# Kernel optimization log

Hardware: AMD Instinct MI355X
Metric: run time of the kernel (lower is better)

The kernel has to match this reference:

```python
import jax, jax.numpy as jnp
import numpy as np

B, T, L = 256, 1024, 64
INIT = 0.1


def setup_inputs() -> dict:
    key = jax.random.key(0)
    k1, k2, k3, k4, k5 = jax.random.split(key, 5)
    scores = jax.random.normal(k1, (B, T, L), dtype=jnp.float32)
    targets = jax.random.randint(k2, (B, T), 0, L)
    start = jax.random.uniform(k3, (L,), dtype=jnp.float32, minval=-INIT, maxval=INIT)
    T_mat = jax.random.uniform(k4, (L, L), dtype=jnp.float32, minval=-INIT, maxval=INIT)
    end = jax.random.uniform(k5, (L,), dtype=jnp.float32, minval=-INIT, maxval=INIT)
    return {"scores": scores, "targets": targets, "start": start, "T_mat": T_mat, "end": end}


def reference(scores, targets, start, T_mat, end):
    # scores: [B,T,L], targets: [B,T] int, start/end: [L], T_mat: [L,L] with T_mat[cur, prev]
    Ttr = T_mat.T  # [prev, cur]

    # --- normalizers via forward algorithm (scan over time) ---
    prev0 = start[None, :] + scores[:, 0]  # [B,L]

    def step(prev, emit):  # prev [B,L], emit [B,L]
        cur = prev[:, :, None] + emit[:, None, :] + Ttr[None, :, :]  # [B,prev,cur]
        return jax.scipy.special.logsumexp(cur, axis=1), None

    emits_t = jnp.swapaxes(scores, 0, 1)[1:]  # [T-1,B,L]
    prev, _ = jax.lax.scan(step, prev0, emits_t)
    normalizers = jax.scipy.special.logsumexp(prev + end[None, :], axis=1)  # [B]

    # --- gold path score ---
    emits = jnp.take_along_axis(scores, targets[:, :, None], axis=2).squeeze(2).sum(axis=1)  # [B]
    trans = (start[targets[:, 0]]
             + T_mat[targets[:, 1:], targets[:, :-1]].sum(axis=1)
             + end[targets[:, -1]])  # [B]
    target_scores = emits + trans

    return (normalizers - target_scores).mean()
```

## Files before the change

### kernel.cpp

```cpp
#include <hip/hip_runtime.h>

#define NB 256
#define NT 1024
#define NL 64

typedef __fp16 h2v __attribute__((ext_vector_type(2)));

__device__ __forceinline__ float rfl_f(float v) {
  return __builtin_bit_cast(float, __builtin_amdgcn_readfirstlane(__builtin_bit_cast(int, v)));
}

__device__ __forceinline__ float dpp_xor1(float v) {
  int i = __builtin_bit_cast(int, v);
  int r = __builtin_amdgcn_update_dpp(i, i, 0xB1, 0xF, 0xF, false);
  return __builtin_bit_cast(float, r);
}

#define DOT4(P, B)                                                            \
  s0 = __builtin_amdgcn_fdot2(__builtin_bit_cast(h2v, (P).x), Rh[(B) + 0], s0, false); \
  s1 = __builtin_amdgcn_fdot2(__builtin_bit_cast(h2v, (P).y), Rh[(B) + 1], s1, false); \
  s2 = __builtin_amdgcn_fdot2(__builtin_bit_cast(h2v, (P).z), Rh[(B) + 2], s2, false); \
  s3 = __builtin_amdgcn_fdot2(__builtin_bit_cast(h2v, (P).w), Rh[(B) + 3], s3, false);

#define CRF_STEP(EF)                                                          \
  do {                                                                        \
    float wn = dpp_xor1(w);                                                   \
    h2v pk = __builtin_amdgcn_cvt_pkrtz(w, wn);                               \
    lb[wslot] = __builtin_bit_cast(int, pk);                                  \
    int4 P0 = lbv[0], P1 = lbv[1], P2 = lbv[2], P3 = lbv[3];                  \
    int4 P4 = lbv[4], P5 = lbv[5], P6 = lbv[6], P7 = lbv[7];                  \
    int e5 = (P0.x >> 10) & 0x1f;                                             \
    float K = __builtin_bit_cast(float, (130 - e5) << 23);                    \
    float KE = K * (EF);                                                      \
    e2 += e5 - 3;                                                             \
    float s0 = 0.f, s1 = 0.f, s2 = 0.f, s3 = 0.f;                             \
    DOT4(P0, 0); DOT4(P1, 4); DOT4(P2, 8); DOT4(P3, 12);                      \
    DOT4(P4, 16); DOT4(P5, 20); DOT4(P6, 24); DOT4(P7, 28);                   \
    w = ((s0 + s1) + (s2 + s3)) * KE;                                         \
  } while (0)

#define AQ __ATOMIC_ACQUIRE
#define RL __ATOMIC_RELEASE
#define SCOPE __HIP_MEMORY_SCOPE_AGENT

__global__ __launch_bounds__(64) void fb_kernel(const float* __restrict__ scores,
                                                const int* __restrict__ targets,
                                                const float* __restrict__ start,
                                                const float* __restrict__ Tm,
                                                const float* __restrict__ endv,
                                                float* __restrict__ wsA,
                                                float* __restrict__ wsG,
                                                float* __restrict__ wsL,
                                                int* __restrict__ flagF,
                                                int* __restrict__ flagG,
                                                int* __restrict__ flagL,
                                                float* __restrict__ out) {
  const int lane = threadIdx.x;
  const int bb = blockIdx.x;

  if (bb >= 2 * NB) {
    const int b = bb - 2 * NB;
    const int* tg = targets + b * NT;
    const float* sc = scores + (size_t)b * NT * NL;
    float acc = 0.f;
    for (int t = lane; t < NT; t += 64) {
      int c = tg[t];
      acc += sc[t * NL + c];
      if (t > 0) acc += Tm[c * NL + tg[t - 1]];
    }
#pragma unroll
    for (int off = 32; off > 0; off >>= 1) acc += __shfl_xor(acc, off, 64);
    if (lane == 0) wsG[b] = acc + start[tg[0]] + endv[tg[NT - 1]];
    __threadfence();
    if (lane == 0) __hip_atomic_store(&flagG[b], 1, RL, SCOPE);
    return;
  }

  __shared__ int4 lbv_s[16];
  int* lb = (int*)lbv_s;
  const int4* lbv = lbv_s;
  const int wslot = (lane & 1) * 32 + (lane >> 1);

  const bool bwd = bb >= NB;
  const int b = bwd ? bb - NB : bb;
  const float* sc = scores + (size_t)b * NT * NL;
  const float LN2 = 0.69314718055994530942f;

  const float* Tb = bwd ? (Tm + lane) : (Tm + lane * NL);
  const int str = bwd ? NL : 1;
  h2v Rh[32];
#pragma unroll
  for (int k = 0; k < 32; k++)
    Rh[k] = __builtin_amdgcn_cvt_pkrtz(__expf(Tb[(2 * k) * str]),
                                       __expf(Tb[(2 * k + 1) * str]));

  if (!bwd) {
    float a0 = start[lane] + sc[lane];
    float m0 = rfl_f(a0);
    float w = __expf(a0 - m0) * 16.f;
    int e2 = -4;

    float buf[4];
#pragma unroll
    for (int k = 0; k < 4; k++) buf[k] = sc[(1 + k) * NL + lane];

    for (int i = 0; i < 128; i++) {
      float nb4[4];
      int tb = 5 + 4 * i;
#pragma unroll
      for (int k = 0; k < 4; k++) nb4[k] = sc[(tb + k) * NL + lane];
      float Ev[4];
#pragma unroll
      for (int k = 0; k < 4; k++) Ev[k] = __expf(buf[k]);
      CRF_STEP(Ev[0]);
      CRF_STEP(Ev[1]);
      CRF_STEP(Ev[2]);
      CRF_STEP(Ev[3]);
#pragma unroll
      for (int k = 0; k < 4; k++) buf[k] = nb4[k];
    }
    wsA[b * NL + lane] = m0 + (float)e2 * LN2 + __logf(w);
    __threadfence();
    if (lane == 0) __hip_atomic_store(&flagF[b], 1, RL, SCOPE);
  } else {
    float a0 = endv[lane] + sc[(NT - 1) * NL + lane];
    float m0 = rfl_f(a0);
    float w = __expf(a0 - m0) * 16.f;
    int e2 = -4;

    float buf[4];
#pragma unroll
    for (int k = 0; k < 4; k++) buf[k] = sc[(1022 - k) * NL + lane];

    for (int i = 0; i < 127; i++) {
      float nb4[4];
      int tb = 1018 - 4 * i;
#pragma unroll
      for (int k = 0; k < 4; k++) nb4[k] = sc[(tb - k) * NL + lane];
      float Ev[4];
#pragma unroll
      for (int k = 0; k < 4; k++) Ev[k] = __expf(buf[k]);
      CRF_STEP(Ev[0]);
      CRF_STEP(Ev[1]);
      CRF_STEP(Ev[2]);
      CRF_STEP(Ev[3]);
#pragma unroll
      for (int k = 0; k < 4; k++) buf[k] = nb4[k];
    }
    CRF_STEP(__expf(sc[514 * NL + lane]));
    CRF_STEP(__expf(sc[513 * NL + lane]));
    CRF_STEP(1.0f);
    float bv = m0 + (float)e2 * LN2 + __logf(w);

    while (__hip_atomic_load(&flagF[b], AQ, SCOPE) == 0) __builtin_amdgcn_s_sleep(2);
    float v = wsA[b * NL + lane] + bv;
    float m = v;
#pragma unroll
    for (int off = 32; off > 0; off >>= 1) m = fmaxf(m, __shfl_xor(m, off, 64));
    float s = __expf(v - m);
#pragma unroll
    for (int off = 32; off > 0; off >>= 1) s += __shfl_xor(s, off, 64);
    while (__hip_atomic_load(&flagG[b], AQ, SCOPE) == 0) __builtin_amdgcn_s_sleep(2);
    float loss = (m + __logf(s)) - wsG[b];

    if (lane == 0) {
      wsL[b] = loss;
      __threadfence();
      __hip_atomic_store(&flagL[b], 1, RL, SCOPE);
    }

    if (b == 0) {
      for (;;) {
        int f0 = __hip_atomic_load(&flagL[lane], AQ, SCOPE);
        int f1 = __hip_atomic_load(&flagL[lane + 64], AQ, SCOPE);
        int f2 = __hip_atomic_load(&flagL[lane + 128], AQ, SCOPE);
        int f3 = __hip_atomic_load(&flagL[lane + 192], AQ, SCOPE);
        if (__all((f0 & f1 & f2 & f3) != 0)) break;
        __builtin_amdgcn_s_sleep(8);
      }
      float t0 = __builtin_bit_cast(float, __hip_atomic_load((int*)&wsL[lane], AQ, SCOPE));
      float t1 = __builtin_bit_cast(float, __hip_atomic_load((int*)&wsL[lane + 64], AQ, SCOPE));
      float t2 = __builtin_bit_cast(float, __hip_atomic_load((int*)&wsL[lane + 128], AQ, SCOPE));
      float t3 = __builtin_bit_cast(float, __hip_atomic_load((int*)&wsL[lane + 192], AQ, SCOPE));
      float tot = (t0 + t1) + (t2 + t3);
#pragma unroll
      for (int off = 32; off > 0; off >>= 1) tot += __shfl_xor(tot, off, 64);
      if (lane == 0) out[0] = tot * (1.0f / NB);
    }
  }
}

extern "C" void kernel_launch(void* const* d_in, const int* in_sizes, int n_in,
                              void* d_out, int out_size, void* d_ws, size_t ws_size,
                              hipStream_t stream) {
  const float* scores = (const float*)d_in[0];
  const int* targets = (const int*)d_in[1];
  const float* start = (const float*)d_in[2];
  const float* Tm = (const float*)d_in[3];
  const float* endv = (const float*)d_in[4];
  float* out = (float*)d_out;

  int* flagF = (int*)d_ws;
  int* flagG = flagF + NB;
  int* flagL = flagG + NB;
  float* wsG = (float*)(flagL + NB + 64);
  float* wsL = wsG + NB;
  float* wsA = wsL + NB;

  hipMemsetAsync(flagF, 0, 3 * NB * sizeof(int), stream);
  fb_kernel<<<3 * NB, 64, 0, stream>>>(scores, targets, start, Tm, endv,
                                       wsA, wsG, wsL, flagF, flagG, flagL, out);
}
```

Measured before the change: 202.6 us.

## Merge forward, backward and gold-score waves into one block per batch

Replaces three separate single-wave blocks per batch element, which were coordinated through global flags, with one 192-thread block. Wave 0 runs the forward pass, wave 1 the backward pass and wave 2 the gold path score, and they combine results through shared memory after a __syncthreads. This removes global-memory spin-waits, workspace round trips and a larger memset. Placing all three waves of a batch element on the same CU may change scheduling and occupancy compared with spreading 768 independent blocks across the device.

After: 204.5 us. About the same (+0.9%).

```diff
diff --git a/kernel.cpp b/kernel.cpp
--- a/kernel.cpp
+++ b/kernel.cpp
@@ -43,125 +43,121 @@
 #define RL __ATOMIC_RELEASE
 #define SCOPE __HIP_MEMORY_SCOPE_AGENT
 
-__global__ __launch_bounds__(64) void fb_kernel(const float* __restrict__ scores,
-                                                const int* __restrict__ targets,
-                                                const float* __restrict__ start,
-                                                const float* __restrict__ Tm,
-                                                const float* __restrict__ endv,
-                                                float* __restrict__ wsA,
-                                                float* __restrict__ wsG,
-                                                float* __restrict__ wsL,
-                                                int* __restrict__ flagF,
-                                                int* __restrict__ flagG,
-                                                int* __restrict__ flagL,
-                                                float* __restrict__ out) {
-  const int lane = threadIdx.x;
-  const int bb = blockIdx.x;
-
-  if (bb >= 2 * NB) {
-    const int b = bb - 2 * NB;
+__global__ __launch_bounds__(192) void fb_kernel(const float* __restrict__ scores,
+                                                 const int* __restrict__ targets,
+                                                 const float* __restrict__ start,
+                                                 const float* __restrict__ Tm,
+                                                 const float* __restrict__ endv,
+                                                 float* __restrict__ wsL,
+                                                 int* __restrict__ flagL,
+                                                 float* __restrict__ out) {
+  const int lane = threadIdx.x & 63;
+  const int wv = threadIdx.x >> 6;
+  const int b = blockIdx.x;
+  const float* sc = scores + (size_t)b * NT * NL;
+  const float LN2 = 0.69314718055994530942f;
+
+  __shared__ int4 lbv_s[2][16];
+  __shared__ float shA[NL];
+  __shared__ float shB[NL];
+  __shared__ float shG;
+
+  if (wv == 2) {
     const int* tg = targets + b * NT;
-    const float* sc = scores + (size_t)b * NT * NL;
     float acc = 0.f;
-    for (int t = lane; t < NT; t += 64) {
+#pragma unroll
+    for (int k = 0; k < 16; k++) {
+      int t = lane + 64 * k;
       int c = tg[t];
       acc += sc[t * NL + c];
       if (t > 0) acc += Tm[c * NL + tg[t - 1]];
     }
 #pragma unroll
     for (int off = 32; off > 0; off >>= 1) acc += __shfl_xor(acc, off, 64);
-    if (lane == 0) wsG[b] = acc + start[tg[0]] + endv[tg[NT - 1]];
-    __threadfence();
-    if (lane == 0) __hip_atomic_store(&flagG[b], 1, RL, SCOPE);
-    return;
+    if (lane == 0) shG = acc + start[tg[0]] + endv[tg[NT - 1]];
+  } else {
+    int* lb = (int*)lbv_s[wv];
+    const int4* lbv = lbv_s[wv];
+    const int wslot = (lane & 1) * 32 + (lane >> 1);
+
+    const bool bwd = wv == 1;
+    const float* Tb = bwd ? (Tm + lane) : (Tm + lane * NL);
+    const int str = bwd ? NL : 1;
+    h2v Rh[32];
+#pragma unroll
+    for (int k = 0; k < 32; k++)
+      Rh[k] = __builtin_amdgcn_cvt_pkrtz(__expf(Tb[(2 * k) * str]),
+                                         __expf(Tb[(2 * k + 1) * str]));
+
+    if (!bwd) {
+      float a0 = start[lane] + sc[lane];
+      float m0 = rfl_f(a0);
+      float w = __expf(a0 - m0) * 16.f;
+      int e2 = -4;
+
+      float buf[4];
+#pragma unroll
+      for (int k = 0; k < 4; k++) buf[k] = sc[(1 + k) * NL + lane];
+
+      for (int i = 0; i < 128; i++) {
+        float nb4[4];
+        int tb = 5 + 4 * i;
+#pragma unroll
+        for (int k = 0; k < 4; k++) nb4[k] = sc[(tb + k) * NL + lane];
+        float Ev[4];
+#pragma unroll
+        for (int k = 0; k < 4; k++) Ev[k] = __expf(buf[k]);
+        CRF_STEP(Ev[0]);
+        CRF_STEP(Ev[1]);
+        CRF_STEP(Ev[2]);
+        CRF_STEP(Ev[3]);
+#pragma unroll
+        for (int k = 0; k < 4; k++) buf[k] = nb4[k];
+      }
+      shA[lane] = m0 + (float)e2 * LN2 + __logf(w);
+    } else {
+      float a0 = endv[lane] + sc[(NT - 1) * NL + lane];
+      float m0 = rfl_f(a0);
+      float w = __expf(a0 - m0) * 16.f;
+      int e2 = -4;
+
+      float buf[4];
+#pragma unroll
+      for (int k = 0; k < 4; k++) buf[k] = sc[(1022 - k) * NL + lane];
+
+      for (int i = 0; i < 127; i++) {
+        float nb4[4];
+        int tb = 1018 - 4 * i;
+#pragma unroll
+        for (int k = 0; k < 4; k++) nb4[k] = sc[(tb - k) * NL + lane];
+        float Ev[4];
+#pragma unroll
+        for (int k = 0; k < 4; k++) Ev[k] = __expf(buf[k]);
+        CRF_STEP(Ev[0]);
+        CRF_STEP(Ev[1]);
+        CRF_STEP(Ev[2]);
+        CRF_STEP(Ev[3]);
+#pragma unroll
+        for (int k = 0; k < 4; k++) buf[k] = nb4[k];
+      }
+      CRF_STEP(__expf(sc[514 * NL + lane]));
+      CRF_STEP(__expf(sc[513 * NL + lane]));
+      CRF_STEP(1.0f);
+      shB[lane] = m0 + (float)e2 * LN2 + __logf(w);
+    }
   }
 
-  __shared__ int4 lbv_s[16];
-  int* lb = (int*)lbv_s;
-  const int4* lbv = lbv_s;
-  const int wslot = (lane & 1) * 32 + (lane >> 1);
-
-  const bool bwd = bb >= NB;
-  const int b = bwd ? bb - NB : bb;
-  const float* sc = scores + (size_t)b * NT * NL;
-  const float LN2 = 0.69314718055994530942f;
-
-  const float* Tb = bwd ? (Tm + lane) : (Tm + lane * NL);
-  const int str = bwd ? NL : 1;
-  h2v Rh[32];
-#pragma unroll
-  for (int k = 0; k < 32; k++)
-    Rh[k] = __builtin_amdgcn_cvt_pkrtz(__expf(Tb[(2 * k) * str]),
-                                       __expf(Tb[(2 * k + 1) * str]));
-
-  if (!bwd) {
-    float a0 = start[lane] + sc[lane];
-    float m0 = rfl_f(a0);
-    float w = __expf(a0 - m0) * 16.f;
-    int e2 = -4;
-
-    float buf[4];
-#pragma unroll
-    for (int k = 0; k < 4; k++) buf[k] = sc[(1 + k) * NL + lane];
-
-    for (int i = 0; i < 128; i++) {
-      float nb4[4];
-      int tb = 5 + 4 * i;
-#pragma unroll
-      for (int k = 0; k < 4; k++) nb4[k] = sc[(tb + k) * NL + lane];
-      float Ev[4];
-#pragma unroll
-      for (int k = 0; k < 4; k++) Ev[k] = __expf(buf[k]);
-      CRF_STEP(Ev[0]);
-      CRF_STEP(Ev[1]);
-      CRF_STEP(Ev[2]);
-      CRF_STEP(Ev[3]);
-#pragma unroll
-      for (int k = 0; k < 4; k++) buf[k] = nb4[k];
-    }
-    wsA[b * NL + lane] = m0 + (float)e2 * LN2 + __logf(w);
-    __threadfence();
-    if (lane == 0) __hip_atomic_store(&flagF[b], 1, RL, SCOPE);
-  } else {
-    float a0 = endv[lane] + sc[(NT - 1) * NL + lane];
-    float m0 = rfl_f(a0);
-    float w = __expf(a0 - m0) * 16.f;
-    int e2 = -4;
-
-    float buf[4];
-#pragma unroll
-    for (int k = 0; k < 4; k++) buf[k] = sc[(1022 - k) * NL + lane];
-
-    for (int i = 0; i < 127; i++) {
-      float nb4[4];
-      int tb = 1018 - 4 * i;
-#pragma unroll
-      for (int k = 0; k < 4; k++) nb4[k] = sc[(tb - k) * NL + lane];
-      float Ev[4];
-#pragma unroll
-      for (int k = 0; k < 4; k++) Ev[k] = __expf(buf[k]);
-      CRF_STEP(Ev[0]);
-      CRF_STEP(Ev[1]);
-      CRF_STEP(Ev[2]);
-      CRF_STEP(Ev[3]);
-#pragma unroll
-      for (int k = 0; k < 4; k++) buf[k] = nb4[k];
-    }
-    CRF_STEP(__expf(sc[514 * NL + lane]));
-    CRF_STEP(__expf(sc[513 * NL + lane]));
-    CRF_STEP(1.0f);
-    float bv = m0 + (float)e2 * LN2 + __logf(w);
-
-    while (__hip_atomic_load(&flagF[b], AQ, SCOPE) == 0) __builtin_amdgcn_s_sleep(2);
-    float v = wsA[b * NL + lane] + bv;
+  __syncthreads();
+
+  if (wv == 0) {
+    float v = shA[lane] + shB[lane];
     float m = v;
 #pragma unroll
     for (int off = 32; off > 0; off >>= 1) m = fmaxf(m, __shfl_xor(m, off, 64));
     float s = __expf(v - m);
 #pragma unroll
     for (int off = 32; off > 0; off >>= 1) s += __shfl_xor(s, off, 64);
-    while (__hip_atomic_load(&flagG[b], AQ, SCOPE) == 0) __builtin_amdgcn_s_sleep(2);
-    float loss = (m + __logf(s)) - wsG[b];
+    float loss = (m + __logf(s)) - shG;
 
     if (lane == 0) {
       wsL[b] = loss;
@@ -200,14 +196,9 @@
   const float* endv = (const float*)d_in[4];
   float* out = (float*)d_out;
 
-  int* flagF = (int*)d_ws;
-  int* flagG = flagF + NB;
-  int* flagL = flagG + NB;
-  float* wsG = (float*)(flagL + NB + 64);
-  float* wsL = wsG + NB;
-  float* wsA = wsL + NB;
-
-  hipMemsetAsync(flagF, 0, 3 * NB * sizeof(int), stream);
-  fb_kernel<<<3 * NB, 64, 0, stream>>>(scores, targets, start, Tm, endv,
-                                       wsA, wsG, wsL, flagF, flagG, flagL, out);
-}
+  int* flagL = (int*)d_ws;
+  float* wsL = (float*)(flagL + NB);
+
+  hipMemsetAsync(flagL, 0, NB * sizeof(int), stream);
+  fb_kernel<<<NB, 192, 0, stream>>>(scores, targets, start, Tm, endv, wsL, flagL, out);
+}
```
